# Performance work log

Measured on AMD Instinct MI355X. Metric: run time of the kernel, lower is better.

## Reference

```python
import jax, jax.numpy as jnp
import numpy as np

B, S, D, H = 4, 2048, 1024, 16
HD = D // H


def setup_inputs() -> dict:
    key = jax.random.key(0)
    ks = jax.random.split(key, 12)
    scale = 1.0 / np.sqrt(D)
    q = jax.random.normal(ks[0], (B, S, D), jnp.float32)
    k = jax.random.normal(ks[1], (B, S, D), jnp.float32)
    v = jax.random.normal(ks[2], (B, S, D), jnp.float32)
    mask = jax.random.randint(ks[3], (B, S, S), 0, 2).astype(bool)
    Wq = jax.random.normal(ks[4], (D, D), jnp.float32) * scale
    bq = jnp.zeros((D,), jnp.float32)
    Wk = jax.random.normal(ks[5], (D, D), jnp.float32) * scale
    bk = jnp.zeros((D,), jnp.float32)
    Wv = jax.random.normal(ks[6], (D, D), jnp.float32) * scale
    bv = jnp.zeros((D,), jnp.float32)
    Wo = jax.random.normal(ks[7], (D, D), jnp.float32) * scale
    bo = jnp.zeros((D,), jnp.float32)
    return {"q": q, "k": k, "v": v, "mask": mask,
            "Wq": Wq, "bq": bq, "Wk": Wk, "bk": bk,
            "Wv": Wv, "bv": bv, "Wo": Wo, "bo": bo}


def reference(q, k, v, mask, Wq, bq, Wk, bk, Wv, bv, Wo, bo):
    # project and split heads: [B,S,D] -> [B,H,S,HD]
    def split_heads(x, W, b):
        y = x @ W + b
        return y.reshape(B, S, H, HD).transpose(0, 2, 1, 3)

    Q = split_heads(q, Wq, bq)
    K = split_heads(k, Wk, bk)
    V = split_heads(v, Wv, bv)
    inv_sqrt_dk = 1.0 / np.sqrt(HD)
    scores = jnp.einsum('bhqd,bhkd->bhqk', Q, K) * inv_sqrt_dk
    scores = jnp.where(mask[:, None, :, :], -1e9, scores)
    attn = jax.nn.softmax(scores, axis=-1)
    ctx = jnp.einsum('bhqk,bhkd->bhqd', attn, V)  # [B,H,S,HD]
    ctx = ctx.transpose(0, 2, 1, 3).reshape(B, S, D)
    return ctx @ Wo + bo
```

## Files before the change

### kernel.cpp

```cpp
#include <hip/hip_runtime.h>
#include <stdint.h>

#define B_ 4
#define S_ 2048
#define D_ 1024
#define H_ 16
#define HD_ 64

typedef __attribute__((ext_vector_type(8))) __bf16          bf16x8;
typedef __attribute__((ext_vector_type(8))) unsigned short  u16x8;
typedef __attribute__((ext_vector_type(4))) float           f32x4;
typedef __attribute__((ext_vector_type(16))) float          f32x16;
typedef unsigned short u16;
typedef unsigned int   u32;
typedef unsigned long long u64;

union BF8 { u16x8 u; bf16x8 b; u32 w[4]; };

__device__ __forceinline__ u16 f2bf(float f) {
  union { float f; uint32_t u; } v; v.f = f;
  uint32_t r = (v.u + 0x7FFFu + ((v.u >> 16) & 1u)) >> 16;
  return (u16)r;
}

__device__ __forceinline__ u32 cvtpk(float lo, float hi) {
  u32 r;
  asm("v_cvt_pk_bf16_f32 %0, %1, %2" : "=v"(r) : "v"(lo), "v"(hi));
  return r;
}

__device__ __forceinline__ void pswap(u32& a, u32& b) {
  asm("v_permlane32_swap_b32 %0, %1" : "+v"(a), "+v"(b));
}

__device__ __forceinline__ float andf(float x, u32 m) {
  union { float f; u32 u; } v; v.f = x; v.u &= m; return v.f;
}

typedef const unsigned int __attribute__((address_space(1)))* gas1_t;
typedef unsigned int __attribute__((address_space(3)))*       las3_t;

__device__ __forceinline__ void gll16(const void* g, void* l) {
  __builtin_amdgcn_global_load_lds((gas1_t)g, (las3_t)l, 16, 0, 0);
}

#define MFMA32(a, b, c) __builtin_amdgcn_mfma_f32_32x32x16_bf16((a), (b), (c), 0, 0, 0)

__global__ __launch_bounds__(256) void prep_k(const float* __restrict__ qi, const float* __restrict__ ki,
                                              const float* __restrict__ vi, u16* __restrict__ oq,
                                              u16* __restrict__ ok, u16* __restrict__ ov,
                                              const float* __restrict__ Wq, const float* __restrict__ Wk,
                                              const float* __restrict__ Wv, const float* __restrict__ Wo,
                                              u16* __restrict__ Tq, u16* __restrict__ Tk,
                                              u16* __restrict__ Tv, u16* __restrict__ To) {
  __shared__ float tile[64][65];
  int blk = blockIdx.x;
  int t = threadIdx.x;
  if (blk < 12288) {
    const float* in; u16* out;
    if (blk < 4096) { in = qi; out = oq; }
    else if (blk < 8192) { in = ki; out = ok; blk -= 4096; }
    else { in = vi; out = ov; blk -= 8192; }
    int i = blk * 256 + t;
    const float4* p = ((const float4*)in) + (size_t)i * 2;
    float4 a = p[0], b = p[1];
    u16x8 o;
    o[0] = f2bf(a.x); o[1] = f2bf(a.y); o[2] = f2bf(a.z); o[3] = f2bf(a.w);
    o[4] = f2bf(b.x); o[5] = f2bf(b.y); o[6] = f2bf(b.z); o[7] = f2bf(b.w);
    *(((u16x8*)out) + i) = o;
    return;
  }
  int wi = blk - 12288;
  int z = wi >> 8, rem = wi & 255;
  int bx = rem & 15, by = rem >> 4;
  const float* src; u16* dst;
  switch (z) {
    case 0: src = Wq; dst = Tq; break;
    case 1: src = Wk; dst = Tk; break;
    case 2: src = Wv; dst = Tv; break;
    default: src = Wo; dst = To; break;
  }
  int k0 = bx * 64, n0 = by * 64;
#pragma unroll
  for (int it = 0; it < 4; ++it) {
    int idx = it * 256 + t;
    int r = idx >> 4, c = idx & 15;
    float4 v = *(const float4*)(src + (size_t)(k0 + r) * 1024 + n0 + c * 4);
    tile[r][c * 4 + 0] = v.x; tile[r][c * 4 + 1] = v.y;
    tile[r][c * 4 + 2] = v.z; tile[r][c * 4 + 3] = v.w;
  }
  __syncthreads();
#pragma unroll
  for (int it = 0; it < 2; ++it) {
    int idx = it * 256 + t;
    int n = idx >> 3, kc = idx & 7;
    u16x8 o;
#pragma unroll
    for (int j = 0; j < 8; ++j) o[j] = f2bf(tile[kc * 8 + j][n]);
    *(u16x8*)(dst + (size_t)(n0 + n) * 1024 + k0 + kc * 8) = o;
  }
}

__global__ __launch_bounds__(256) void vtmask_k(const u16* __restrict__ Vh, u16* __restrict__ Vt,
                                                const void* __restrict__ mraw, u64* __restrict__ mout) {
  __shared__ u16 tile[64][66];
  int blk = blockIdx.x;
  int t = threadIdx.x;
  if (blk < 2048) {
    int s0 = (blk & 31) * 64, bh = blk >> 5;
    const u16* src = Vh + ((size_t)bh * S_ + s0) * HD_;
#pragma unroll
    for (int i = 0; i < 2; ++i) {
      int idx = i * 256 + t;
      int r = idx >> 3, c = idx & 7;
      u16x8 v = *(const u16x8*)(src + (size_t)r * HD_ + c * 8);
#pragma unroll
      for (int j = 0; j < 8; ++j) tile[r][c * 8 + j] = v[j];
    }
    __syncthreads();
    u16* dst = Vt + (size_t)bh * HD_ * S_ + s0;
#pragma unroll
    for (int i = 0; i < 2; ++i) {
      int idx = i * 256 + t;
      int hd = idx >> 3, c = idx & 7;
      u16x8 o;
#pragma unroll
      for (int j = 0; j < 8; ++j) o[j] = tile[c * 8 + j][hd];
      *(u16x8*)(dst + (size_t)hd * S_ + c * 8) = o;
    }
    return;
  }
  const u32* hdr = (const u32*)mraw;
  int lane = t & 63;
  u32 hv = hdr[lane];
  bool isf = (hv == 0x3F800000u);
  u64 bigm = __ballot(hv > 1u && !isf);
  u64 fm = __ballot(isf);
  int fmt = (__popcll(fm) > 8) ? 2 : ((bigm != 0ull) ? 0 : 1);
  size_t idx = (size_t)(blk - 2048) * 256 + t;
  u64 bits = 0;
  if (fmt == 0) {
    const u64* p = (const u64*)((const uint8_t*)mraw + idx * 64);
#pragma unroll
    for (int j = 0; j < 8; ++j) {
      u64 v = p[j];
#pragma unroll
      for (int kk = 0; kk < 8; ++kk)
        bits |= (u64)(((v >> (8 * kk)) & 0xFFull) != 0) << (j * 8 + kk);
    }
  } else if (fmt == 1) {
    const int* p = ((const int*)mraw) + idx * 64;
#pragma unroll
    for (int j = 0; j < 64; ++j) bits |= (u64)(p[j] != 0) << j;
  } else {
    const u32* p = ((const u32*)mraw) + idx * 64;
#pragma unroll
    for (int j = 0; j < 64; ++j) bits |= (u64)((p[j] << 1) != 0) << j;
  }
  mout[idx] = bits;
}

__global__ __launch_bounds__(256) void proj3_k(const u16* __restrict__ Aq, const u16* __restrict__ Ak,
                                               const u16* __restrict__ Av,
                                               const u16* __restrict__ Tq, const u16* __restrict__ Tk,
                                               const u16* __restrict__ Tv,
                                               const float* __restrict__ bq, const float* __restrict__ bk,
                                               const float* __restrict__ bv,
                                               u16* __restrict__ Qh, u16* __restrict__ Kh,
                                               u16* __restrict__ Vh, float qscale) {
  int g = blockIdx.x >> 9, bid = blockIdx.x & 511;
  const u16* A; const u16* Bt; const float* bias; u16* outp; float scale;
  if (g == 0) { A = Aq; Bt = Tq; bias = bq; outp = Qh; scale = qscale; }
  else if (g == 1) { A = Ak; Bt = Tk; bias = bk; outp = Kh; scale = 1.0f; }
  else { A = Av; Bt = Tv; bias = bv; outp = Vh; scale = 1.0f; }
  int xcd = bid & 7, loc = bid >> 3;
  int mt = xcd * 8 + (loc & 7), nt = loc >> 3;
  int m0 = mt * 128, n0 = nt * 128;
  int t = threadIdx.x, w = t >> 6, lane = t & 63;
  int l15 = lane & 15, l4 = lane >> 4;
  int wm = w >> 1, wn = w & 1;
  __shared__ __align__(16) char smem[16384];
  const f32x4 vzero = {0.f, 0.f, 0.f, 0.f};
  f32x4 acc[4][4];
#pragma unroll
  for (int a = 0; a < 4; ++a)
#pragma unroll
    for (int c = 0; c < 4; ++c) acc[a][c] = vzero;

  for (int k0 = 0; k0 < 1024; k0 += 32) {
#pragma unroll
    for (int i = 0; i < 2; ++i) {
      int chunk = i * 256 + w * 64 + lane;
      int row = chunk >> 2, slot = chunk & 3;
      int sc = slot ^ ((row >> 1) & 3);
      gll16(A + (size_t)(m0 + row) * 1024 + k0 + sc * 8, smem + (i * 256 + w * 64) * 16);
      gll16(Bt + (size_t)(n0 + row) * 1024 + k0 + sc * 8, smem + 8192 + (i * 256 + w * 64) * 16);
    }
    __syncthreads();
    BF8 am[4], bn[4];
#pragma unroll
    for (int mb = 0; mb < 4; ++mb) {
      int row = wm * 64 + mb * 16 + l15;
      int sl = l4 ^ ((row >> 1) & 3);
      am[mb].u = *(const u16x8*)(smem + row * 64 + sl * 16);
    }
#pragma unroll
    for (int nb = 0; nb < 4; ++nb) {
      int row = wn * 64 + nb * 16 + l15;
      int sl = l4 ^ ((row >> 1) & 3);
      bn[nb].u = *(const u16x8*)(smem + 8192 + row * 64 + sl * 16);
    }
#pragma unroll
    for (int mb = 0; mb < 4; ++mb)
#pragma unroll
      for (int nb = 0; nb < 4; ++nb)
        acc[mb][nb] = __builtin_amdgcn_mfma_f32_16x16x32_bf16(am[mb].b, bn[nb].b, acc[mb][nb], 0, 0, 0);
    __syncthreads();
  }
#pragma unroll
  for (int mb = 0; mb < 4; ++mb)
#pragma unroll
    for (int nb = 0; nb < 4; ++nb)
#pragma unroll
      for (int r = 0; r < 4; ++r) {
        int grow = m0 + wm * 64 + mb * 16 + l4 * 4 + r;
        int gcol = n0 + wn * 64 + nb * 16 + l15;
        float v = (acc[mb][nb][r] + bias[gcol]) * scale;
        int bb = grow >> 11, s = grow & 2047, h = gcol >> 6, hd = gcol & 63;
        outp[(((size_t)bb * H_ + h) * S_ + s) * HD_ + hd] = f2bf(v);
      }
}

__global__ __launch_bounds__(256) void gemmo_k(const u16* __restrict__ A,
                                               const u16* __restrict__ Bt,
                                               const float* __restrict__ bias,
                                               float* __restrict__ outp) {
  int bid = blockIdx.x;
  int xcd = bid & 7, loc = bid >> 3;
  int mt = xcd * 8 + (loc & 7), nt = loc >> 3;
  int m0 = mt * 128, n0 = nt * 128;
  int t = threadIdx.x, w = t >> 6, lane = t & 63;
  int l15 = lane & 15, l4 = lane >> 4;
  int wm = w >> 1, wn = w & 1;
  __shared__ __align__(16) char smem[16384];
  const f32x4 vzero = {0.f, 0.f, 0.f, 0.f};
  f32x4 acc[4][4];
#pragma unroll
  for (int a = 0; a < 4; ++a)
#pragma unroll
    for (int c = 0; c < 4; ++c) acc[a][c] = vzero;

  for (int k0 = 0; k0 < 1024; k0 += 32) {
#pragma unroll
    for (int i = 0; i < 2; ++i) {
      int chunk = i * 256 + w * 64 + lane;
      int row = chunk >> 2, slot = chunk & 3;
      int sc = slot ^ ((row >> 1) & 3);
      gll16(A + (size_t)(m0 + row) * 1024 + k0 + sc * 8, smem + (i * 256 + w * 64) * 16);
      gll16(Bt + (size_t)(n0 + row) * 1024 + k0 + sc * 8, smem + 8192 + (i * 256 + w * 64) * 16);
    }
    __syncthreads();
    BF8 am[4], bn[4];
#pragma unroll
    for (int mb = 0; mb < 4; ++mb) {
      int row = wm * 64 + mb * 16 + l15;
      int sl = l4 ^ ((row >> 1) & 3);
      am[mb].u = *(const u16x8*)(smem + row * 64 + sl * 16);
    }
#pragma unroll
    for (int nb = 0; nb < 4; ++nb) {
      int row = wn * 64 + nb * 16 + l15;
      int sl = l4 ^ ((row >> 1) & 3);
      bn[nb].u = *(const u16x8*)(smem + 8192 + row * 64 + sl * 16);
    }
#pragma unroll
    for (int mb = 0; mb < 4; ++mb)
#pragma unroll
      for (int nb = 0; nb < 4; ++nb)
        acc[mb][nb] = __builtin_amdgcn_mfma_f32_16x16x32_bf16(am[mb].b, bn[nb].b, acc[mb][nb], 0, 0, 0);
    __syncthreads();
  }
#pragma unroll
  for (int mb = 0; mb < 4; ++mb)
#pragma unroll
    for (int nb = 0; nb < 4; ++nb)
#pragma unroll
      for (int r = 0; r < 4; ++r) {
        int grow = m0 + wm * 64 + mb * 16 + l4 * 4 + r;
        int gcol = n0 + wn * 64 + nb * 16 + l15;
        outp[(size_t)grow * 1024 + gcol] = acc[mb][nb][r] + bias[gcol];
      }
}

__global__ __launch_bounds__(256) void flash_k(const u16* __restrict__ Qh,
                                               const u16* __restrict__ Kh,
                                               const u16* __restrict__ Vt,
                                               const u64* __restrict__ mb,
                                               u16* __restrict__ ctx) {
  int bid = blockIdx.x;
  int xcd = bid & 7, loc = bid >> 3;
  int bh = xcd * 8 + (loc & 7);
  int qblk = loc >> 3;
  int b = bh >> 4, h = bh & 15;
  int t = threadIdx.x, w = t >> 6, lane = t & 63;
  int l31 = lane & 31, l5 = lane >> 5;
  __shared__ __align__(16) char smem[32768];

  int q0 = qblk * 128 + w * 32;
  const u16* kbase = Kh + (size_t)bh * S_ * HD_;
  const u16* vbase = Vt + (size_t)bh * HD_ * S_;
  const uint2* mrow = ((const uint2*)mb) + ((size_t)b * S_ + q0 + l31) * 32;

  const u16* qbase = Qh + ((size_t)bh * S_ + q0 + l31) * HD_;
  BF8 qf[4];
#pragma unroll
  for (int dk = 0; dk < 4; ++dk) qf[dk].u = *(const u16x8*)(qbase + dk * 16 + l5 * 8);

  int koff0[4], koffB[4];
#pragma unroll
  for (int dk = 0; dk < 4; ++dk) {
    int s0_ = (dk * 2 + l5) ^ (l31 & 7) ^ (l31 >> 3);
    koff0[dk] = l31 * 128 + s0_ * 16;
    koffB[dk] = 4096 + l31 * 128 + ((s0_ ^ 4) * 16);
  }

  BF8 onesf;
#pragma unroll
  for (int i = 0; i < 8; ++i) onesf.u[i] = 0x3F80;

  f32x16 o0, o1, lac;
#pragma unroll
  for (int r = 0; r < 16; ++r) { o0[r] = 0.f; o1[r] = 0.f; lac[r] = 0.f; }

#define STAGE(KT, BUF)                                                          \
  do {                                                                          \
    char* Kd = smem + (BUF);                                                    \
    int k0s = (KT) * 64;                                                        \
    _Pragma("unroll") for (int i_ = 0; i_ < 2; ++i_) {                          \
      int c_ = i_ * 256 + t;                                                    \
      int row_ = c_ >> 3, sl_ = c_ & 7;                                         \
      int sc_ = sl_ ^ (row_ & 7) ^ (row_ >> 3);                                 \
      int cw_ = (i_ * 256 + w * 64) * 16;                                       \
      gll16(kbase + (size_t)(k0s + row_) * HD_ + sc_ * 8, Kd + cw_);            \
      gll16(vbase + (size_t)row_ * S_ + k0s + sc_ * 8, Kd + 8192 + cw_);        \
    }                                                                           \
  } while (0)

#define MKFRAG(FR, A0, B0, C0, D0)                                              \
  do {                                                                          \
    u32 xx0 = (A0), xx1 = (C0), yy0 = (B0), yy1 = (D0);                         \
    pswap(xx0, xx1); pswap(yy0, yy1);                                           \
    FR.w[0] = xx0; FR.w[1] = yy0; FR.w[2] = xx1; FR.w[3] = yy1;                 \
  } while (0)

#define PVS(FR, KC)                                                             \
  do {                                                                          \
    lac = MFMA32(FR.b, onesf.b, lac);                                           \
    BF8 vf0, vf1;                                                               \
    vf0.u = *(const u16x8*)(Kb + 8192 + koff0[(KC)]);                           \
    vf1.u = *(const u16x8*)(Kb + 8192 + koffB[(KC)]);                           \
    o0 = MFMA32(FR.b, vf0.b, o0);                                               \
    o1 = MFMA32(FR.b, vf1.b, o1);                                               \
  } while (0)

#define FTILE(KT, BUF, OBUF, ISLAST)                                            \
  {                                                                             \
    __syncthreads();                                                            \
    uint2 mw = mrow[(KT)];                                                      \
    if (!(ISLAST)) STAGE((KT) + 1, OBUF);                                       \
    const char* Kb = smem + (BUF);                                              \
    f32x16 sa0, sa1;                                                            \
    _Pragma("unroll") for (int r = 0; r < 16; ++r) { sa0[r] = 0.f; sa1[r] = 0.f; } \
    __builtin_amdgcn_s_setprio(1);                                              \
    _Pragma("unroll") for (int dk = 0; dk < 4; ++dk) {                          \
      BF8 kf0, kf1;                                                             \
      kf0.u = *(const u16x8*)(Kb + koff0[dk]);                                  \
      kf1.u = *(const u16x8*)(Kb + koffB[dk]);                                  \
      sa0 = MFMA32(kf0.b, qf[dk].b, sa0);                                       \
      sa1 = MFMA32(kf1.b, qf[dk].b, sa1);                                       \
    }                                                                           \
    __builtin_amdgcn_s_setprio(0);                                              \
    u32 nw0 = ~(mw.x >> (l5 * 4));                                              \
    u32 nw1 = ~(mw.y >> (l5 * 4));                                              \
    _Pragma("unroll") for (int r = 0; r < 16; ++r) {                            \
      const int pp = (r & 3) + 8 * (r >> 2);                                    \
      sa0[r] = andf(exp2f(sa0[r]), (u32)__builtin_amdgcn_sbfe((int)nw0, pp, 1));\
      sa1[r] = andf(exp2f(sa1[r]), (u32)__builtin_amdgcn_sbfe((int)nw1, pp, 1));\
    }                                                                           \
    u32 pk0[8], pk1[8];                                                         \
    _Pragma("unroll") for (int i = 0; i < 8; ++i) {                             \
      pk0[i] = cvtpk(sa0[2 * i], sa0[2 * i + 1]);                               \
      pk1[i] = cvtpk(sa1[2 * i], sa1[2 * i + 1]);                               \
    }                                                                           \
    BF8 fr0, fr1, fr2, fr3;                                                     \
    MKFRAG(fr0, pk0[0], pk0[1], pk0[2], pk0[3]);                                \
    MKFRAG(fr1, pk0[4], pk0[5], pk0[6], pk0[7]);                                \
    MKFRAG(fr2, pk1[0], pk1[1], pk1[2], pk1[3]);                                \
    MKFRAG(fr3, pk1[4], pk1[5], pk1[6], pk1[7]);                                \
    __builtin_amdgcn_s_setprio(1);                                              \
    PVS(fr0, 0); PVS(fr1, 1); PVS(fr2, 2); PVS(fr3, 3);                         \
    __builtin_amdgcn_s_setprio(0);                                              \
  }

  STAGE(0, 0);
  for (int kt2 = 0; kt2 < 16; ++kt2) {
    FTILE(2 * kt2, 0, 16384, false);
    FTILE(2 * kt2 + 1, 16384, 0, (kt2 == 15));
  }

#pragma unroll
  for (int r = 0; r < 16; ++r) {
    float inv = 1.f / (lac[r] + 1e-35f);
    int q = (r & 3) + 8 * (r >> 2) + 4 * l5;
    size_t base = ((size_t)b * S_ + q0 + q) * D_ + h * HD_;
    ctx[base + l31]      = f2bf(o0[r] * inv);
    ctx[base + 32 + l31] = f2bf(o1[r] * inv);
  }
#undef STAGE
#undef MKFRAG
#undef PVS
#undef FTILE
}

extern "C" void kernel_launch(void* const* d_in, const int* in_sizes, int n_in,
                              void* d_out, int out_size, void* d_ws, size_t ws_size,
                              hipStream_t stream) {
  (void)in_sizes; (void)n_in; (void)out_size; (void)ws_size;
  const float* q  = (const float*)d_in[0];
  const float* k  = (const float*)d_in[1];
  const float* v  = (const float*)d_in[2];
  const void*  mk = d_in[3];
  const float* Wq = (const float*)d_in[4];
  const float* bq = (const float*)d_in[5];
  const float* Wk = (const float*)d_in[6];
  const float* bk = (const float*)d_in[7];
  const float* Wv = (const float*)d_in[8];
  const float* bv = (const float*)d_in[9];
  const float* Wo = (const float*)d_in[10];
  const float* bo = (const float*)d_in[11];

  char* ws = (char*)d_ws;
  u16* qb   = (u16*)(ws + 0);
  u16* kbuf = (u16*)(ws + 16777216);
  u16* vbuf = (u16*)(ws + 33554432);
  u16* Tq   = (u16*)(ws + 50331648);
  u16* Tk   = (u16*)(ws + 52428800);
  u16* Tv   = (u16*)(ws + 54525952);
  u16* To   = (u16*)(ws + 56623104);
  u16* Qh   = (u16*)(ws + 58720256);
  u16* Kh   = (u16*)(ws + 75497472);
  u16* Vh   = (u16*)(ws + 92274688);
  u16* Vt   = qb;
  u16* ctx  = kbuf;
  u64* mc   = (u64*)vbuf;

  const float QSCALE = 0.18033688011112042f;

  prep_k<<<13312, 256, 0, stream>>>(q, k, v, qb, kbuf, vbuf,
                                    Wq, Wk, Wv, Wo, Tq, Tk, Tv, To);
  proj3_k<<<1536, 256, 0, stream>>>(qb, kbuf, vbuf, Tq, Tk, Tv,
                                    bq, bk, bv, Qh, Kh, Vh, QSCALE);
  vtmask_k<<<3072, 256, 0, stream>>>(Vh, Vt, mk, mc);
  flash_k<<<1024, 256, 0, stream>>>(Qh, Kh, Vt, mc, ctx);
  gemmo_k<<<512, 256, 0, stream>>>(ctx, To, bo, (float*)d_out);
}
```

Measured before the change: 286.3 us.

## Write V projection directly in transposed layout, drop separate V transpose pass

The V projection epilogue now stores bf16 results straight into the head-transposed [B,H,HD,S] layout using 4-element vector stores. This removes the V transpose blocks from the mask-packing kernel, which now only packs the mask. It saves a full read and write of V in bf16 and shrinks the launch grid. The flash kernel also seeds its first QK MFMA from a zero vector instead of zeroing the accumulators each tile.

```diff
diff --git a/kernel.cpp b/kernel.cpp
--- a/kernel.cpp
+++ b/kernel.cpp
@@ -9,6 +9,7 @@
 
 typedef __attribute__((ext_vector_type(8))) __bf16          bf16x8;
 typedef __attribute__((ext_vector_type(8))) unsigned short  u16x8;
+typedef __attribute__((ext_vector_type(4))) unsigned short  u16x4;
 typedef __attribute__((ext_vector_type(4))) float           f32x4;
 typedef __attribute__((ext_vector_type(16))) float          f32x16;
 typedef unsigned short u16;
@@ -101,43 +102,17 @@
   }
 }
 
-__global__ __launch_bounds__(256) void vtmask_k(const u16* __restrict__ Vh, u16* __restrict__ Vt,
-                                                const void* __restrict__ mraw, u64* __restrict__ mout) {
-  __shared__ u16 tile[64][66];
-  int blk = blockIdx.x;
+__global__ __launch_bounds__(256) void maskpack_k(const void* __restrict__ mraw,
+                                                  u64* __restrict__ mout) {
+  const u32* hdr = (const u32*)mraw;
   int t = threadIdx.x;
-  if (blk < 2048) {
-    int s0 = (blk & 31) * 64, bh = blk >> 5;
-    const u16* src = Vh + ((size_t)bh * S_ + s0) * HD_;
-#pragma unroll
-    for (int i = 0; i < 2; ++i) {
-      int idx = i * 256 + t;
-      int r = idx >> 3, c = idx & 7;
-      u16x8 v = *(const u16x8*)(src + (size_t)r * HD_ + c * 8);
-#pragma unroll
-      for (int j = 0; j < 8; ++j) tile[r][c * 8 + j] = v[j];
-    }
-    __syncthreads();
-    u16* dst = Vt + (size_t)bh * HD_ * S_ + s0;
-#pragma unroll
-    for (int i = 0; i < 2; ++i) {
-      int idx = i * 256 + t;
-      int hd = idx >> 3, c = idx & 7;
-      u16x8 o;
-#pragma unroll
-      for (int j = 0; j < 8; ++j) o[j] = tile[c * 8 + j][hd];
-      *(u16x8*)(dst + (size_t)hd * S_ + c * 8) = o;
-    }
-    return;
-  }
-  const u32* hdr = (const u32*)mraw;
   int lane = t & 63;
   u32 hv = hdr[lane];
   bool isf = (hv == 0x3F800000u);
   u64 bigm = __ballot(hv > 1u && !isf);
   u64 fm = __ballot(isf);
   int fmt = (__popcll(fm) > 8) ? 2 : ((bigm != 0ull) ? 0 : 1);
-  size_t idx = (size_t)(blk - 2048) * 256 + t;
+  size_t idx = (size_t)blockIdx.x * 256 + t;
   u64 bits = 0;
   if (fmt == 0) {
     const u64* p = (const u64*)((const uint8_t*)mraw + idx * 64);
@@ -167,12 +142,12 @@
                                                const float* __restrict__ bq, const float* __restrict__ bk,
                                                const float* __restrict__ bv,
                                                u16* __restrict__ Qh, u16* __restrict__ Kh,
-                                               u16* __restrict__ Vh, float qscale) {
+                                               u16* __restrict__ Vt, float qscale) {
   int g = blockIdx.x >> 9, bid = blockIdx.x & 511;
   const u16* A; const u16* Bt; const float* bias; u16* outp; float scale;
   if (g == 0) { A = Aq; Bt = Tq; bias = bq; outp = Qh; scale = qscale; }
   else if (g == 1) { A = Ak; Bt = Tk; bias = bk; outp = Kh; scale = 1.0f; }
-  else { A = Av; Bt = Tv; bias = bv; outp = Vh; scale = 1.0f; }
+  else { A = Av; Bt = Tv; bias = bv; outp = Vt; scale = 1.0f; }
   int xcd = bid & 7, loc = bid >> 3;
   int mt = xcd * 8 + (loc & 7), nt = loc >> 3;
   int m0 = mt * 128, n0 = nt * 128;
@@ -217,18 +192,35 @@
         acc[mb][nb] = __builtin_amdgcn_mfma_f32_16x16x32_bf16(am[mb].b, bn[nb].b, acc[mb][nb], 0, 0, 0);
     __syncthreads();
   }
-#pragma unroll
-  for (int mb = 0; mb < 4; ++mb)
-#pragma unroll
-    for (int nb = 0; nb < 4; ++nb)
-#pragma unroll
-      for (int r = 0; r < 4; ++r) {
-        int grow = m0 + wm * 64 + mb * 16 + l4 * 4 + r;
-        int gcol = n0 + wn * 64 + nb * 16 + l15;
-        float v = (acc[mb][nb][r] + bias[gcol]) * scale;
-        int bb = grow >> 11, s = grow & 2047, h = gcol >> 6, hd = gcol & 63;
-        outp[(((size_t)bb * H_ + h) * S_ + s) * HD_ + hd] = f2bf(v);
+  if (g == 2) {
+#pragma unroll
+    for (int mb = 0; mb < 4; ++mb)
+#pragma unroll
+      for (int nb = 0; nb < 4; ++nb) {
+        int no = n0 + wn * 64 + nb * 16 + l15;
+        int h = no >> 6, hd = no & 63;
+        int m = m0 + wm * 64 + mb * 16 + l4 * 4;
+        int bb = m >> 11, s = m & 2047;
+        float bsv = bias[no];
+        u16x4 ov;
+#pragma unroll
+        for (int r = 0; r < 4; ++r) ov[r] = f2bf(acc[mb][nb][r] + bsv);
+        *(u16x4*)(outp + (((size_t)bb * H_ + h) * HD_ + hd) * S_ + s) = ov;
       }
+  } else {
+#pragma unroll
+    for (int mb = 0; mb < 4; ++mb)
+#pragma unroll
+      for (int nb = 0; nb < 4; ++nb)
+#pragma unroll
+        for (int r = 0; r < 4; ++r) {
+          int grow = m0 + wm * 64 + mb * 16 + l4 * 4 + r;
+          int gcol = n0 + wn * 64 + nb * 16 + l15;
+          float v = (acc[mb][nb][r] + bias[gcol]) * scale;
+          int bb = grow >> 11, s = grow & 2047, h = gcol >> 6, hd = gcol & 63;
+          outp[(((size_t)bb * H_ + h) * S_ + s) * HD_ + hd] = f2bf(v);
+        }
+  }
 }
 
 __global__ __launch_bounds__(256) void gemmo_k(const u16* __restrict__ A,
@@ -328,9 +320,9 @@
 #pragma unroll
   for (int i = 0; i < 8; ++i) onesf.u[i] = 0x3F80;
 
-  f32x16 o0, o1, lac;
-#pragma unroll
-  for (int r = 0; r < 16; ++r) { o0[r] = 0.f; o1[r] = 0.f; lac[r] = 0.f; }
+  f32x16 o0, o1, lac, zv;
+#pragma unroll
+  for (int r = 0; r < 16; ++r) { o0[r] = 0.f; o1[r] = 0.f; lac[r] = 0.f; zv[r] = 0.f; }
 
 #define STAGE(KT, BUF)                                                          \
   do {                                                                          \
@@ -370,9 +362,15 @@
     if (!(ISLAST)) STAGE((KT) + 1, OBUF);                                       \
     const char* Kb = smem + (BUF);                                              \
     f32x16 sa0, sa1;                                                            \
-    _Pragma("unroll") for (int r = 0; r < 16; ++r) { sa0[r] = 0.f; sa1[r] = 0.f; } \
     __builtin_amdgcn_s_setprio(1);                                              \
-    _Pragma("unroll") for (int dk = 0; dk < 4; ++dk) {                          \
+    {                                                                           \
+      BF8 kf0, kf1;                                                             \
+      kf0.u = *(const u16x8*)(Kb + koff0[0]);                                   \
+      kf1.u = *(const u16x8*)(Kb + koffB[0]);                                   \
+      sa0 = MFMA32(kf0.b, qf[0].b, zv);                                         \
+      sa1 = MFMA32(kf1.b, qf[0].b, zv);                                         \
+    }                                                                           \
+    _Pragma("unroll") for (int dk = 1; dk < 4; ++dk) {                          \
       BF8 kf0, kf1;                                                             \
       kf0.u = *(const u16x8*)(Kb + koff0[dk]);                                  \
       kf1.u = *(const u16x8*)(Kb + koffB[dk]);                                  \
@@ -449,8 +447,7 @@
   u16* To   = (u16*)(ws + 56623104);
   u16* Qh   = (u16*)(ws + 58720256);
   u16* Kh   = (u16*)(ws + 75497472);
-  u16* Vh   = (u16*)(ws + 92274688);
-  u16* Vt   = qb;
+  u16* Vt   = (u16*)(ws + 92274688);
   u16* ctx  = kbuf;
   u64* mc   = (u64*)vbuf;
 
@@ -459,8 +456,8 @@
   prep_k<<<13312, 256, 0, stream>>>(q, k, v, qb, kbuf, vbuf,
                                     Wq, Wk, Wv, Wo, Tq, Tk, Tv, To);
   proj3_k<<<1536, 256, 0, stream>>>(qb, kbuf, vbuf, Tq, Tk, Tv,
-                                    bq, bk, bv, Qh, Kh, Vh, QSCALE);
-  vtmask_k<<<3072, 256, 0, stream>>>(Vh, Vt, mk, mc);
+                                    bq, bk, bv, Qh, Kh, Vt, QSCALE);
+  maskpack_k<<<1024, 256, 0, stream>>>(mk, mc);
   flash_k<<<1024, 256, 0, stream>>>(Qh, Kh, Vt, mc, ctx);
   gemmo_k<<<512, 256, 0, stream>>>(ctx, To, bo, (float*)d_out);
 }
```

After: 279.5 us. 1.02x faster.
